# Performance work log

Hardware: AMD Instinct MI355X
Metric: run time of the kernel (lower is better)

The kernel has to match this reference:

```python
import jax, jax.numpy as jnp
import numpy as np

N, E, T = 32768, 262144, 262144
DN, DE = 128, 128
EPS = 1e-5  # torch LayerNorm default eps


def layer_norm(x, g, b):
    m = jnp.mean(x, axis=-1, keepdims=True)
    v = jnp.mean((x - m) ** 2, axis=-1, keepdims=True)
    return (x - m) * jax.lax.rsqrt(v + EPS) * g + b


def setup_inputs() -> dict:
    key = jax.random.key(0)
    ks = jax.random.split(key, 16)
    node_embedding = jax.random.normal(ks[0], (N, DN), dtype=jnp.float32)
    edge_embedding = jax.random.normal(ks[1], (E, DE), dtype=jnp.float32)
    i = jax.random.randint(ks[2], (E,), 0, N)
    j = jax.random.randint(ks[3], (E,), 0, N)
    index_i = jax.random.randint(ks[4], (T,), 0, N)
    index_j = jax.random.randint(ks[5], (T,), 0, N)
    index_k = jax.random.randint(ks[6], (T,), 0, N)
    index_ji = jax.random.randint(ks[7], (T,), 0, E)
    index_kj = jax.random.randint(ks[8], (T,), 0, E)
    d3 = 3 * DN + 2 * DE
    W2 = jax.random.normal(ks[9], (2 * DE, DN), dtype=jnp.float32) / np.sqrt(DN)
    b2 = jnp.zeros((2 * DE,), dtype=jnp.float32)
    W3 = jax.random.normal(ks[10], (2 * DE, d3), dtype=jnp.float32) / np.sqrt(d3)
    b3 = jnp.zeros((2 * DE,), dtype=jnp.float32)
    g_c2 = jnp.ones((2 * DE,), jnp.float32); be_c2 = jnp.zeros((2 * DE,), jnp.float32)
    g_c3 = jnp.ones((2 * DE,), jnp.float32); be_c3 = jnp.zeros((2 * DE,), jnp.float32)
    g_c2_2 = jnp.ones((DE,), jnp.float32); be_c2_2 = jnp.zeros((DE,), jnp.float32)
    g_c3_2 = jnp.ones((DE,), jnp.float32); be_c3_2 = jnp.zeros((DE,), jnp.float32)
    return dict(node_embedding=node_embedding, edge_embedding=edge_embedding,
                i=i, j=j, index_i=index_i, index_j=index_j, index_k=index_k,
                index_ji=index_ji, index_kj=index_kj,
                W2=W2, b2=b2, W3=W3, b3=b3,
                g_c2=g_c2, be_c2=be_c2, g_c3=g_c3, be_c3=be_c3,
                g_c2_2=g_c2_2, be_c2_2=be_c2_2, g_c3_2=g_c3_2, be_c3_2=be_c3_2)


def reference(node_embedding, edge_embedding, i, j, index_i, index_j, index_k,
              index_ji, index_kj, W2, b2, W3, b3,
              g_c2, be_c2, g_c3, be_c3, g_c2_2, be_c2_2, g_c3_2, be_c3_2):
    num_edges = edge_embedding.shape[0]
    # --- c2 branch: per-edge elementwise product of endpoint node embeddings ---
    c2 = node_embedding[i] * node_embedding[j]                      # [E, Dn]
    c2 = layer_norm(c2 @ W2.T + b2, g_c2, be_c2)                    # [E, 2De]
    c2_filter, c2_core = jnp.split(c2, 2, axis=1)
    c2_emb = layer_norm(jax.nn.sigmoid(c2_filter) * jnp.tanh(c2_core), g_c2_2, be_c2_2)
    # --- c3 branch: triplet gather -> linear -> LN -> gate -> scatter-sum ---
    c3 = jnp.concatenate([node_embedding[index_i], node_embedding[index_j],
                          node_embedding[index_k], edge_embedding[index_ji],
                          edge_embedding[index_kj]], axis=1)        # [T, 3Dn+2De]
    c3 = layer_norm(c3 @ W3.T + b3, g_c3, be_c3)                    # [T, 2De]
    c3_filter, c3_core = jnp.split(c3, 2, axis=1)
    msg = jax.nn.sigmoid(c3_filter) * jnp.tanh(c3_core)             # [T, De]
    c3_emb = jax.ops.segment_sum(msg, index_ji, num_segments=num_edges)  # [E, De]
    c3_emb = layer_norm(c3_emb, g_c3_2, be_c3_2)
    return jnp.tanh(edge_embedding + c2_emb + c3_emb)
```

## Files before the change

### kernel.cpp

```cpp
#include <hip/hip_runtime.h>

typedef _Float16 h16;
typedef _Float16 h16x8 __attribute__((ext_vector_type(8)));
typedef float    f32x4 __attribute__((ext_vector_type(4)));

static constexpr int NN  = 32768;
static constexpr int EE  = 262144;
static constexpr int TT  = 262144;
static constexpr int D   = 128;
static constexpr int K3  = 640;
static constexpr int LDA = 72;
#define EPS 1e-5f

__global__ __launch_bounds__(256) void cvt_f32_f16(
    const float* __restrict__ src, h16* __restrict__ dst, int n8)
{
    const int i = blockIdx.x * 256 + threadIdx.x;
    if (i >= n8) return;
    const float4* s = reinterpret_cast<const float4*>(src);
    const float4 a = s[2 * i], b = s[2 * i + 1];
    h16x8 o;
    o[0] = (h16)a.x; o[1] = (h16)a.y; o[2] = (h16)a.z; o[3] = (h16)a.w;
    o[4] = (h16)b.x; o[5] = (h16)b.y; o[6] = (h16)b.z; o[7] = (h16)b.w;
    *reinterpret_cast<h16x8*>(dst + 8 * i) = o;
}

__global__ __launch_bounds__(256, 2) void c3_kernel(
    const h16*  __restrict__ nodeh, const float* __restrict__ edge,
    const h16*  __restrict__ edgeh,
    const int* __restrict__ idx_i, const int* __restrict__ idx_j,
    const int* __restrict__ idx_k, const int* __restrict__ idx_ji,
    const int* __restrict__ idx_kj,
    const h16* __restrict__ W3h, const float* __restrict__ b3,
    const float* __restrict__ g3, const float* __restrict__ be3,
    float* __restrict__ acc3)
{
    __shared__ h16 As[128 * LDA];
    __shared__ h16 Bs[256 * LDA];

    const int tid  = threadIdx.x;
    const int lane = tid & 63;
    const int wave = tid >> 6;
    const int l15  = lane & 15;
    const int quad = lane >> 4;
    const int m0   = blockIdx.x * 128;

    f32x4 acc[2][16];
    #pragma unroll
    for (int mt = 0; mt < 2; ++mt)
        #pragma unroll
        for (int nt = 0; nt < 16; ++nt)
            acc[mt][nt] = (f32x4){0.f, 0.f, 0.f, 0.f};

    const int r = tid >> 1;
    const int h = tid & 1;

    const size_t rI  = (size_t)idx_i [m0 + r];
    const size_t rJ  = (size_t)idx_j [m0 + r];
    const size_t rK  = (size_t)idx_k [m0 + r];
    const size_t rJI = (size_t)idx_ji[m0 + r];
    const size_t rKJ = (size_t)idx_kj[m0 + r];

    h16x8 av[4], bv[8];

#define LDC3(c)                                                                          \
    {                                                                                    \
        const int seg  = (c) >> 1;                                                       \
        const int half = (c) & 1;                                                        \
        const size_t row = (seg == 0) ? rI : (seg == 1) ? rJ                             \
                         : (seg == 2) ? rK : (seg == 3) ? rJI : rKJ;                     \
        if (seg < 3) {                                                                   \
            const h16x8* sp = reinterpret_cast<const h16x8*>(                            \
                nodeh + row * D + half * 64 + h * 32);                                   \
            _Pragma("unroll")                                                            \
            for (int q = 0; q < 4; ++q) av[q] = sp[q];                                   \
        } else if (edgeh) {                                                              \
            const h16x8* sp = reinterpret_cast<const h16x8*>(                            \
                edgeh + row * D + half * 64 + h * 32);                                   \
            _Pragma("unroll")                                                            \
            for (int q = 0; q < 4; ++q) av[q] = sp[q];                                   \
        } else {                                                                         \
            const float4* fp = reinterpret_cast<const float4*>(                          \
                edge + row * D + half * 64 + h * 32);                                    \
            _Pragma("unroll")                                                            \
            for (int q = 0; q < 4; ++q) {                                                \
                const float4 u = fp[2 * q], vv = fp[2 * q + 1];                          \
                h16x8 t;                                                                 \
                t[0] = (h16)u.x;  t[1] = (h16)u.y;  t[2] = (h16)u.z;  t[3] = (h16)u.w;   \
                t[4] = (h16)vv.x; t[5] = (h16)vv.y; t[6] = (h16)vv.z; t[7] = (h16)vv.w;  \
                av[q] = t;                                                               \
            }                                                                            \
        }                                                                                \
        const h16x8* wp = reinterpret_cast<const h16x8*>(                                \
            W3h + (size_t)tid * K3 + (c) * 64);                                          \
        _Pragma("unroll")                                                                \
        for (int q = 0; q < 8; ++q) bv[q] = wp[q];                                       \
    }

    LDC3(0);

    #pragma unroll 1
    for (int c = 0; c < 10; ++c) {
        __syncthreads();
        h16x8* ad = reinterpret_cast<h16x8*>(&As[r * LDA + h * 32]);
        #pragma unroll
        for (int q = 0; q < 4; ++q) ad[q] = av[q];
        h16x8* bd = reinterpret_cast<h16x8*>(&Bs[tid * LDA]);
        #pragma unroll
        for (int q = 0; q < 8; ++q) bd[q] = bv[q];
        __syncthreads();

        if (c < 9) LDC3(c + 1);

        #pragma unroll
        for (int kk = 0; kk < 64; kk += 32) {
            h16x8 a0 = *reinterpret_cast<const h16x8*>(&As[(wave*32      + l15) * LDA + kk + quad*8]);
            h16x8 a1 = *reinterpret_cast<const h16x8*>(&As[(wave*32 + 16 + l15) * LDA + kk + quad*8]);
            #pragma unroll
            for (int nt = 0; nt < 16; ++nt) {
                h16x8 b = *reinterpret_cast<const h16x8*>(&Bs[(nt*16 + l15) * LDA + kk + quad*8]);
                acc[0][nt] = __builtin_amdgcn_mfma_f32_16x16x32_f16(a0, b, acc[0][nt], 0, 0, 0);
                acc[1][nt] = __builtin_amdgcn_mfma_f32_16x16x32_f16(a1, b, acc[1][nt], 0, 0, 0);
            }
        }
    }
#undef LDC3

    float bias[16], gg[16], bb[16];
    #pragma unroll
    for (int nt = 0; nt < 16; ++nt) {
        const int cc = nt * 16 + l15;
        bias[nt] = b3[cc]; gg[nt] = g3[cc]; bb[nt] = be3[cc];
    }
    #pragma unroll
    for (int mt = 0; mt < 2; ++mt) {
        #pragma unroll
        for (int rg = 0; rg < 4; ++rg) {
            float v[16];
            float s = 0.f, s2 = 0.f;
            #pragma unroll
            for (int nt = 0; nt < 16; ++nt) {
                v[nt] = acc[mt][nt][rg] + bias[nt];
                s += v[nt]; s2 += v[nt] * v[nt];
            }
            #pragma unroll
            for (int m = 1; m < 16; m <<= 1) {
                s  += __shfl_xor(s,  m, 64);
                s2 += __shfl_xor(s2, m, 64);
            }
            const float mean = s * (1.f / 256.f);
            const float var  = s2 * (1.f / 256.f) - mean * mean;
            const float inv  = rsqrtf(var + EPS);
            const int rowg   = m0 + wave * 32 + mt * 16 + quad * 4 + rg;
            const size_t e   = (size_t)idx_ji[rowg];
            #pragma unroll
            for (int nt = 0; nt < 8; ++nt) {
                const float f   = (v[nt]     - mean) * inv * gg[nt]     + bb[nt];
                const float co  = (v[nt + 8] - mean) * inv * gg[nt + 8] + bb[nt + 8];
                const float msg = (1.f / (1.f + __expf(-f))) * tanhf(co);
                atomicAdd(&acc3[e * D + nt * 16 + l15], msg);
            }
        }
    }
}

__global__ __launch_bounds__(256, 2) void c2_kernel(
    const h16* __restrict__ nodeh,
    const int* __restrict__ ei, const int* __restrict__ ej,
    const h16* __restrict__ W2h, const float* __restrict__ b2,
    const float* __restrict__ g2, const float* __restrict__ be2,
    const float* __restrict__ g22, const float* __restrict__ be22,
    h16* __restrict__ c2emb)
{
    __shared__ h16 As[128 * LDA];
    __shared__ h16 Bs[256 * LDA];

    const int tid  = threadIdx.x;
    const int lane = tid & 63;
    const int wave = tid >> 6;
    const int l15  = lane & 15;
    const int quad = lane >> 4;
    const int m0   = blockIdx.x * 128;

    f32x4 acc[2][16];
    #pragma unroll
    for (int mt = 0; mt < 2; ++mt)
        #pragma unroll
        for (int nt = 0; nt < 16; ++nt)
            acc[mt][nt] = (f32x4){0.f, 0.f, 0.f, 0.f};

    const int r = tid >> 1;
    const int h = tid & 1;
    const size_t ri = (size_t)ei[m0 + r];
    const size_t rj = (size_t)ej[m0 + r];

    h16x8 av[4], bv[8];

#define LDC2(c)                                                                          \
    {                                                                                    \
        const h16x8* si = reinterpret_cast<const h16x8*>(                                \
            nodeh + ri * D + (c) * 64 + h * 32);                                         \
        const h16x8* sj = reinterpret_cast<const h16x8*>(                                \
            nodeh + rj * D + (c) * 64 + h * 32);                                         \
        _Pragma("unroll")                                                                \
        for (int q = 0; q < 4; ++q) av[q] = si[q] * sj[q];                               \
        const h16x8* wp = reinterpret_cast<const h16x8*>(                                \
            W2h + (size_t)tid * D + (c) * 64);                                           \
        _Pragma("unroll")                                                                \
        for (int q = 0; q < 8; ++q) bv[q] = wp[q];                                       \
    }

    LDC2(0);

    #pragma unroll 1
    for (int c = 0; c < 2; ++c) {
        __syncthreads();
        h16x8* ad = reinterpret_cast<h16x8*>(&As[r * LDA + h * 32]);
        #pragma unroll
        for (int q = 0; q < 4; ++q) ad[q] = av[q];
        h16x8* bd = reinterpret_cast<h16x8*>(&Bs[tid * LDA]);
        #pragma unroll
        for (int q = 0; q < 8; ++q) bd[q] = bv[q];
        __syncthreads();

        if (c < 1) LDC2(c + 1);

        #pragma unroll
        for (int kk = 0; kk < 64; kk += 32) {
            h16x8 a0 = *reinterpret_cast<const h16x8*>(&As[(wave*32      + l15) * LDA + kk + quad*8]);
            h16x8 a1 = *reinterpret_cast<const h16x8*>(&As[(wave*32 + 16 + l15) * LDA + kk + quad*8]);
            #pragma unroll
            for (int nt = 0; nt < 16; ++nt) {
                h16x8 b = *reinterpret_cast<const h16x8*>(&Bs[(nt*16 + l15) * LDA + kk + quad*8]);
                acc[0][nt] = __builtin_amdgcn_mfma_f32_16x16x32_f16(a0, b, acc[0][nt], 0, 0, 0);
                acc[1][nt] = __builtin_amdgcn_mfma_f32_16x16x32_f16(a1, b, acc[1][nt], 0, 0, 0);
            }
        }
    }
#undef LDC2

    float bias[16], gg[16], bb[16];
    #pragma unroll
    for (int nt = 0; nt < 16; ++nt) {
        const int cc = nt * 16 + l15;
        bias[nt] = b2[cc]; gg[nt] = g2[cc]; bb[nt] = be2[cc];
    }
    float g2c[8], b2c[8];
    #pragma unroll
    for (int nt = 0; nt < 8; ++nt) {
        const int cc = nt * 16 + l15;
        g2c[nt] = g22[cc]; b2c[nt] = be22[cc];
    }
    #pragma unroll
    for (int mt = 0; mt < 2; ++mt) {
        #pragma unroll
        for (int rg = 0; rg < 4; ++rg) {
            float v[16];
            float s = 0.f, s2 = 0.f;
            #pragma unroll
            for (int nt = 0; nt < 16; ++nt) {
                v[nt] = acc[mt][nt][rg] + bias[nt];
                s += v[nt]; s2 += v[nt] * v[nt];
            }
            #pragma unroll
            for (int m = 1; m < 16; m <<= 1) {
                s  += __shfl_xor(s,  m, 64);
                s2 += __shfl_xor(s2, m, 64);
            }
            const float mean = s * (1.f / 256.f);
            const float var  = s2 * (1.f / 256.f) - mean * mean;
            const float inv  = rsqrtf(var + EPS);
            float msg[8];
            float t = 0.f, t2 = 0.f;
            #pragma unroll
            for (int nt = 0; nt < 8; ++nt) {
                const float f  = (v[nt]     - mean) * inv * gg[nt]     + bb[nt];
                const float co = (v[nt + 8] - mean) * inv * gg[nt + 8] + bb[nt + 8];
                const float m_ = (1.f / (1.f + __expf(-f))) * tanhf(co);
                msg[nt] = m_; t += m_; t2 += m_ * m_;
            }
            #pragma unroll
            for (int m = 1; m < 16; m <<= 1) {
                t  += __shfl_xor(t,  m, 64);
                t2 += __shfl_xor(t2, m, 64);
            }
            const float mean2 = t * (1.f / 128.f);
            const float var2  = t2 * (1.f / 128.f) - mean2 * mean2;
            const float inv2  = rsqrtf(var2 + EPS);
            const size_t rowg = (size_t)(m0 + wave * 32 + mt * 16 + quad * 4 + rg);
            #pragma unroll
            for (int nt = 0; nt < 8; ++nt) {
                const float o = (msg[nt] - mean2) * inv2 * g2c[nt] + b2c[nt];
                c2emb[rowg * D + nt * 16 + l15] = (h16)o;
            }
        }
    }
}

__global__ __launch_bounds__(256) void final_kernel(
    const float* __restrict__ edge, const h16* __restrict__ c2emb,
    const float* __restrict__ g32, const float* __restrict__ be32,
    float* out)
{
    const int lane = threadIdx.x & 63;
    const int wave = threadIdx.x >> 6;
    const size_t e = (size_t)blockIdx.x * 4 + wave;
    const int c0 = lane * 2;

    const float2 v = *reinterpret_cast<const float2*>(&out[e * D + c0]);
    float s  = v.x + v.y;
    float s2 = v.x * v.x + v.y * v.y;
    #pragma unroll
    for (int m = 1; m < 64; m <<= 1) {
        s  += __shfl_xor(s,  m, 64);
        s2 += __shfl_xor(s2, m, 64);
    }
    const float mean = s * (1.f / 128.f);
    const float var  = s2 * (1.f / 128.f) - mean * mean;
    const float inv  = rsqrtf(var + EPS);
    const float c3a = (v.x - mean) * inv * g32[c0]     + be32[c0];
    const float c3b = (v.y - mean) * inv * g32[c0 + 1] + be32[c0 + 1];

    const float2 ev = *reinterpret_cast<const float2*>(&edge[e * D + c0]);
    const float ca = (float)c2emb[e * D + c0];
    const float cb = (float)c2emb[e * D + c0 + 1];
    float2 o;
    o.x = tanhf(ev.x + ca + c3a);
    o.y = tanhf(ev.y + cb + c3b);
    *reinterpret_cast<float2*>(&out[e * D + c0]) = o;
}

extern "C" void kernel_launch(void* const* d_in, const int* in_sizes, int n_in,
                              void* d_out, int out_size, void* d_ws, size_t ws_size,
                              hipStream_t stream)
{
    const float* node   = (const float*)d_in[0];
    const float* edge   = (const float*)d_in[1];
    const int*   e_i    = (const int*)d_in[2];
    const int*   e_j    = (const int*)d_in[3];
    const int*   idx_i  = (const int*)d_in[4];
    const int*   idx_j  = (const int*)d_in[5];
    const int*   idx_k  = (const int*)d_in[6];
    const int*   idx_ji = (const int*)d_in[7];
    const int*   idx_kj = (const int*)d_in[8];
    const float* W2     = (const float*)d_in[9];
    const float* b2     = (const float*)d_in[10];
    const float* W3     = (const float*)d_in[11];
    const float* b3     = (const float*)d_in[12];
    const float* g_c2   = (const float*)d_in[13];
    const float* be_c2  = (const float*)d_in[14];
    const float* g_c3   = (const float*)d_in[15];
    const float* be_c3  = (const float*)d_in[16];
    const float* g_c22  = (const float*)d_in[17];
    const float* be_c22 = (const float*)d_in[18];
    const float* g_c32  = (const float*)d_in[19];
    const float* be_c32 = (const float*)d_in[20];

    h16* W3h   = (h16*)d_ws;
    h16* W2h   = W3h + 256 * K3;
    h16* nodeh = W2h + 256 * D;
    h16* c2emb = nodeh + (size_t)NN * D;
    h16* edgeh = c2emb + (size_t)EE * D;
    const size_t need = ((size_t)256 * K3 + 256 * D + (size_t)NN * D
                         + 2 * (size_t)EE * D) * sizeof(h16);
    const bool use_edgeh = ws_size >= need;

    float* acc3 = (float*)d_out;
    float* out  = (float*)d_out;

    hipMemsetAsync(d_out, 0, (size_t)EE * D * sizeof(float), stream);
    cvt_f32_f16<<<dim3((256 * K3 / 8 + 255) / 256), dim3(256), 0, stream>>>(W3, W3h, 256 * K3 / 8);
    cvt_f32_f16<<<dim3((256 * D  / 8 + 255) / 256), dim3(256), 0, stream>>>(W2, W2h, 256 * D / 8);
    cvt_f32_f16<<<dim3((NN * D   / 8 + 255) / 256), dim3(256), 0, stream>>>(node, nodeh, NN * D / 8);
    if (use_edgeh)
        cvt_f32_f16<<<dim3((EE * D / 8 + 255) / 256), dim3(256), 0, stream>>>(edge, edgeh, EE * D / 8);

    c3_kernel<<<dim3(TT / 128), dim3(256), 0, stream>>>(
        nodeh, edge, use_edgeh ? edgeh : (const h16*)nullptr,
        idx_i, idx_j, idx_k, idx_ji, idx_kj, W3h, b3, g_c3, be_c3, acc3);
    c2_kernel<<<dim3(EE / 128), dim3(256), 0, stream>>>(
        nodeh, e_i, e_j, W2h, b2, g_c2, be_c2, g_c22, be_c22, c2emb);
    final_kernel<<<dim3(EE / 4), dim3(256), 0, stream>>>(
        edge, c2emb, g_c32, be_c32, out);
}
```

Before: 688.9 us.

## Retile c3 MFMA warps as 2x2 and fuse final epilogue into c2 kernel

The c3 GEMM now splits its 4 waves as 2 along M by 2 along N, each covering 64 rows and 128 columns. This raises A-fragment reuse and reduces LDS reads of B per MFMA. The LayerNorm row statistics are combined across the two N-waves through a small shared buffer and an extra barrier. Separately, the final LayerNorm plus tanh stage is folded into the c2 kernel's epilogue. This removes the fp16 c2emb round trip through global memory and one kernel launch, at the cost of more registers and strided per-lane global loads of edge and acc3 in that epilogue.

```diff
diff --git a/kernel.cpp b/kernel.cpp
--- a/kernel.cpp
+++ b/kernel.cpp
@@ -37,19 +37,22 @@
 {
     __shared__ h16 As[128 * LDA];
     __shared__ h16 Bs[256 * LDA];
+    __shared__ float2 Ps[128][2];
 
     const int tid  = threadIdx.x;
     const int lane = tid & 63;
     const int wave = tid >> 6;
+    const int wm   = wave >> 1;
+    const int wn   = wave & 1;
     const int l15  = lane & 15;
     const int quad = lane >> 4;
     const int m0   = blockIdx.x * 128;
 
-    f32x4 acc[2][16];
-    #pragma unroll
-    for (int mt = 0; mt < 2; ++mt)
-        #pragma unroll
-        for (int nt = 0; nt < 16; ++nt)
+    f32x4 acc[4][8];
+    #pragma unroll
+    for (int mt = 0; mt < 4; ++mt)
+        #pragma unroll
+        for (int nt = 0; nt < 8; ++nt)
             acc[mt][nt] = (f32x4){0.f, 0.f, 0.f, 0.f};
 
     const int r = tid >> 1;
@@ -114,51 +117,73 @@
 
         #pragma unroll
         for (int kk = 0; kk < 64; kk += 32) {
-            h16x8 a0 = *reinterpret_cast<const h16x8*>(&As[(wave*32      + l15) * LDA + kk + quad*8]);
-            h16x8 a1 = *reinterpret_cast<const h16x8*>(&As[(wave*32 + 16 + l15) * LDA + kk + quad*8]);
-            #pragma unroll
-            for (int nt = 0; nt < 16; ++nt) {
-                h16x8 b = *reinterpret_cast<const h16x8*>(&Bs[(nt*16 + l15) * LDA + kk + quad*8]);
-                acc[0][nt] = __builtin_amdgcn_mfma_f32_16x16x32_f16(a0, b, acc[0][nt], 0, 0, 0);
-                acc[1][nt] = __builtin_amdgcn_mfma_f32_16x16x32_f16(a1, b, acc[1][nt], 0, 0, 0);
+            h16x8 a[4];
+            #pragma unroll
+            for (int mt = 0; mt < 4; ++mt)
+                a[mt] = *reinterpret_cast<const h16x8*>(
+                    &As[(wm*64 + mt*16 + l15) * LDA + kk + quad*8]);
+            #pragma unroll
+            for (int nt = 0; nt < 8; ++nt) {
+                const int p = (nt < 4) ? (wn*4 + nt) : (8 + wn*4 + nt - 4);
+                h16x8 b = *reinterpret_cast<const h16x8*>(
+                    &Bs[(p*16 + l15) * LDA + kk + quad*8]);
+                #pragma unroll
+                for (int mt = 0; mt < 4; ++mt)
+                    acc[mt][nt] = __builtin_amdgcn_mfma_f32_16x16x32_f16(a[mt], b, acc[mt][nt], 0, 0, 0);
             }
         }
     }
 #undef LDC3
 
-    float bias[16], gg[16], bb[16];
-    #pragma unroll
-    for (int nt = 0; nt < 16; ++nt) {
-        const int cc = nt * 16 + l15;
-        bias[nt] = b3[cc]; gg[nt] = g3[cc]; bb[nt] = be3[cc];
-    }
-    #pragma unroll
-    for (int mt = 0; mt < 2; ++mt) {
+    float bias[2][4], gg[2][4], bb[2][4];
+    #pragma unroll
+    for (int hf = 0; hf < 2; ++hf)
+        #pragma unroll
+        for (int q = 0; q < 4; ++q) {
+            const int cc = hf*128 + (wn*4 + q)*16 + l15;
+            bias[hf][q] = b3[cc]; gg[hf][q] = g3[cc]; bb[hf][q] = be3[cc];
+        }
+
+    float sA[4][4], s2A[4][4];
+    #pragma unroll
+    for (int mt = 0; mt < 4; ++mt) {
         #pragma unroll
         for (int rg = 0; rg < 4; ++rg) {
-            float v[16];
             float s = 0.f, s2 = 0.f;
             #pragma unroll
-            for (int nt = 0; nt < 16; ++nt) {
-                v[nt] = acc[mt][nt][rg] + bias[nt];
-                s += v[nt]; s2 += v[nt] * v[nt];
+            for (int nt = 0; nt < 8; ++nt) {
+                const float x = acc[mt][nt][rg] + bias[nt >> 2][nt & 3];
+                s += x; s2 += x * x;
             }
             #pragma unroll
             for (int m = 1; m < 16; m <<= 1) {
                 s  += __shfl_xor(s,  m, 64);
                 s2 += __shfl_xor(s2, m, 64);
             }
-            const float mean = s * (1.f / 256.f);
-            const float var  = s2 * (1.f / 256.f) - mean * mean;
+            sA[mt][rg] = s; s2A[mt][rg] = s2;
+            if (l15 == 0)
+                Ps[wm*64 + mt*16 + quad*4 + rg][wn] = make_float2(s, s2);
+        }
+    }
+    __syncthreads();
+    #pragma unroll
+    for (int mt = 0; mt < 4; ++mt) {
+        #pragma unroll
+        for (int rg = 0; rg < 4; ++rg) {
+            const int rl = wm*64 + mt*16 + quad*4 + rg;
+            const float2 po = Ps[rl][wn ^ 1];
+            const float S  = sA[mt][rg]  + po.x;
+            const float S2 = s2A[mt][rg] + po.y;
+            const float mean = S * (1.f / 256.f);
+            const float var  = S2 * (1.f / 256.f) - mean * mean;
             const float inv  = rsqrtf(var + EPS);
-            const int rowg   = m0 + wave * 32 + mt * 16 + quad * 4 + rg;
-            const size_t e   = (size_t)idx_ji[rowg];
-            #pragma unroll
-            for (int nt = 0; nt < 8; ++nt) {
-                const float f   = (v[nt]     - mean) * inv * gg[nt]     + bb[nt];
-                const float co  = (v[nt + 8] - mean) * inv * gg[nt + 8] + bb[nt + 8];
+            const size_t e   = (size_t)idx_ji[m0 + rl];
+            #pragma unroll
+            for (int q = 0; q < 4; ++q) {
+                const float f   = (acc[mt][q][rg]     + bias[0][q] - mean) * inv * gg[0][q] + bb[0][q];
+                const float co  = (acc[mt][4 + q][rg] + bias[1][q] - mean) * inv * gg[1][q] + bb[1][q];
                 const float msg = (1.f / (1.f + __expf(-f))) * tanhf(co);
-                atomicAdd(&acc3[e * D + nt * 16 + l15], msg);
+                atomicAdd(&acc3[e * D + (wn*4 + q)*16 + l15], msg);
             }
         }
     }
@@ -170,7 +195,9 @@
     const h16* __restrict__ W2h, const float* __restrict__ b2,
     const float* __restrict__ g2, const float* __restrict__ be2,
     const float* __restrict__ g22, const float* __restrict__ be22,
-    h16* __restrict__ c2emb)
+    const float* __restrict__ g32, const float* __restrict__ be32,
+    const float* __restrict__ edge,
+    float* __restrict__ out)
 {
     __shared__ h16 As[128 * LDA];
     __shared__ h16 Bs[256 * LDA];
@@ -245,11 +272,12 @@
         const int cc = nt * 16 + l15;
         bias[nt] = b2[cc]; gg[nt] = g2[cc]; bb[nt] = be2[cc];
     }
-    float g2c[8], b2c[8];
+    float g2c[8], b2c[8], g3c[8], b3c[8];
     #pragma unroll
     for (int nt = 0; nt < 8; ++nt) {
         const int cc = nt * 16 + l15;
         g2c[nt] = g22[cc]; b2c[nt] = be22[cc];
+        g3c[nt] = g32[cc]; b3c[nt] = be32[cc];
     }
     #pragma unroll
     for (int mt = 0; mt < 2; ++mt) {
@@ -270,64 +298,42 @@
             const float mean = s * (1.f / 256.f);
             const float var  = s2 * (1.f / 256.f) - mean * mean;
             const float inv  = rsqrtf(var + EPS);
-            float msg[8];
-            float t = 0.f, t2 = 0.f;
+            const size_t rowg = (size_t)(m0 + wave * 32 + mt * 16 + quad * 4 + rg);
+
+            float msg[8], a3[8];
+            float t = 0.f, t2 = 0.f, u = 0.f, u2 = 0.f;
             #pragma unroll
             for (int nt = 0; nt < 8; ++nt) {
                 const float f  = (v[nt]     - mean) * inv * gg[nt]     + bb[nt];
                 const float co = (v[nt + 8] - mean) * inv * gg[nt + 8] + bb[nt + 8];
                 const float m_ = (1.f / (1.f + __expf(-f))) * tanhf(co);
                 msg[nt] = m_; t += m_; t2 += m_ * m_;
+                const float a_ = out[rowg * D + nt * 16 + l15];
+                a3[nt] = a_; u += a_; u2 += a_ * a_;
             }
             #pragma unroll
             for (int m = 1; m < 16; m <<= 1) {
                 t  += __shfl_xor(t,  m, 64);
                 t2 += __shfl_xor(t2, m, 64);
+                u  += __shfl_xor(u,  m, 64);
+                u2 += __shfl_xor(u2, m, 64);
             }
             const float mean2 = t * (1.f / 128.f);
             const float var2  = t2 * (1.f / 128.f) - mean2 * mean2;
             const float inv2  = rsqrtf(var2 + EPS);
-            const size_t rowg = (size_t)(m0 + wave * 32 + mt * 16 + quad * 4 + rg);
+            const float mean3 = u * (1.f / 128.f);
+            const float var3  = u2 * (1.f / 128.f) - mean3 * mean3;
+            const float inv3  = rsqrtf(var3 + EPS);
             #pragma unroll
             for (int nt = 0; nt < 8; ++nt) {
-                const float o = (msg[nt] - mean2) * inv2 * g2c[nt] + b2c[nt];
-                c2emb[rowg * D + nt * 16 + l15] = (h16)o;
-            }
-        }
-    }
-}
-
-__global__ __launch_bounds__(256) void final_kernel(
-    const float* __restrict__ edge, const h16* __restrict__ c2emb,
-    const float* __restrict__ g32, const float* __restrict__ be32,
-    float* out)
-{
-    const int lane = threadIdx.x & 63;
-    const int wave = threadIdx.x >> 6;
-    const size_t e = (size_t)blockIdx.x * 4 + wave;
-    const int c0 = lane * 2;
-
-    const float2 v = *reinterpret_cast<const float2*>(&out[e * D + c0]);
-    float s  = v.x + v.y;
-    float s2 = v.x * v.x + v.y * v.y;
-    #pragma unroll
-    for (int m = 1; m < 64; m <<= 1) {
-        s  += __shfl_xor(s,  m, 64);
-        s2 += __shfl_xor(s2, m, 64);
-    }
-    const float mean = s * (1.f / 128.f);
-    const float var  = s2 * (1.f / 128.f) - mean * mean;
-    const float inv  = rsqrtf(var + EPS);
-    const float c3a = (v.x - mean) * inv * g32[c0]     + be32[c0];
-    const float c3b = (v.y - mean) * inv * g32[c0 + 1] + be32[c0 + 1];
-
-    const float2 ev = *reinterpret_cast<const float2*>(&edge[e * D + c0]);
-    const float ca = (float)c2emb[e * D + c0];
-    const float cb = (float)c2emb[e * D + c0 + 1];
-    float2 o;
-    o.x = tanhf(ev.x + ca + c3a);
-    o.y = tanhf(ev.y + cb + c3b);
-    *reinterpret_cast<float2*>(&out[e * D + c0]) = o;
+                const int cc = nt * 16 + l15;
+                const float c2v = (msg[nt] - mean2) * inv2 * g2c[nt] + b2c[nt];
+                const float c3v = (a3[nt]  - mean3) * inv3 * g3c[nt] + b3c[nt];
+                const float ev  = edge[rowg * D + cc];
+                out[rowg * D + cc] = tanhf(ev + c2v + c3v);
+            }
+        }
+    }
 }
 
 extern "C" void kernel_launch(void* const* d_in, const int* in_sizes, int n_in,
@@ -359,10 +365,9 @@
     h16* W3h   = (h16*)d_ws;
     h16* W2h   = W3h + 256 * K3;
     h16* nodeh = W2h + 256 * D;
-    h16* c2emb = nodeh + (size_t)NN * D;
-    h16* edgeh = c2emb + (size_t)EE * D;
+    h16* edgeh = nodeh + (size_t)NN * D;
     const size_t need = ((size_t)256 * K3 + 256 * D + (size_t)NN * D
-                         + 2 * (size_t)EE * D) * sizeof(h16);
+                         + (size_t)EE * D) * sizeof(h16);
     const bool use_edgeh = ws_size >= need;
 
     float* acc3 = (float*)d_out;
@@ -379,7 +384,6 @@
         nodeh, edge, use_edgeh ? edgeh : (const h16*)nullptr,
         idx_i, idx_j, idx_k, idx_ji, idx_kj, W3h, b3, g_c3, be_c3, acc3);
     c2_kernel<<<dim3(EE / 128), dim3(256), 0, stream>>>(
-        nodeh, e_i, e_j, W2h, b2, g_c2, be_c2, g_c22, be_c22, c2emb);
-    final_kernel<<<dim3(EE / 4), dim3(256), 0, stream>>>(
-        edge, c2emb, g_c32, be_c32, out);
+        nodeh, e_i, e_j, W2h, b2, g_c2, be_c2, g_c22, be_c22,
+        g_c32, be_c32, edge, out);
 }
```

Result: slower. 800.9 us (+16.3%).

## Fuse final LayerNorm/tanh into c2 kernel and coalesce gather/weight loads

Applied to the files above, without the earlier changes.

Removes the separate final kernel by folding the c3 LayerNorm, edge add and tanh epilogue into the c2 kernel, which drops the fp16 c2emb intermediate and its write and read. Gather loads now use 8 threads per row with 16-byte chunks, so each row read is a contiguous 128-byte segment. Weights are pre-transposed into a chunk-major layout so that each weight load across threads is coalesced. The c2 epilogue now does extra strided reads of the accumulator and of the edge rows, which may raise register pressure.

```diff
diff --git a/kernel.cpp b/kernel.cpp
--- a/kernel.cpp
+++ b/kernel.cpp
@@ -25,13 +25,32 @@
     *reinterpret_cast<h16x8*>(dst + 8 * i) = o;
 }
 
+__global__ __launch_bounds__(256) void cvt_w_t(
+    const float* __restrict__ src, h16* __restrict__ dst, int K, int n8)
+{
+    const int t = blockIdx.x * 256 + threadIdx.x;
+    if (t >= n8) return;
+    const int d   = t * 8;
+    const int c   = d >> 14;
+    const int rem = d & 16383;
+    const int q   = rem >> 11;
+    const int n   = (rem >> 3) & 255;
+    const int k   = c * 64 + q * 8;
+    const float4* s = reinterpret_cast<const float4*>(src + (size_t)n * K + k);
+    const float4 a = s[0], b = s[1];
+    h16x8 o;
+    o[0] = (h16)a.x; o[1] = (h16)a.y; o[2] = (h16)a.z; o[3] = (h16)a.w;
+    o[4] = (h16)b.x; o[5] = (h16)b.y; o[6] = (h16)b.z; o[7] = (h16)b.w;
+    *reinterpret_cast<h16x8*>(dst + d) = o;
+}
+
 __global__ __launch_bounds__(256, 2) void c3_kernel(
     const h16*  __restrict__ nodeh, const float* __restrict__ edge,
     const h16*  __restrict__ edgeh,
     const int* __restrict__ idx_i, const int* __restrict__ idx_j,
     const int* __restrict__ idx_k, const int* __restrict__ idx_ji,
     const int* __restrict__ idx_kj,
-    const h16* __restrict__ W3h, const float* __restrict__ b3,
+    const h16* __restrict__ W3t, const float* __restrict__ b3,
     const float* __restrict__ g3, const float* __restrict__ be3,
     float* __restrict__ acc3)
 {
@@ -52,14 +71,18 @@
         for (int nt = 0; nt < 16; ++nt)
             acc[mt][nt] = (f32x4){0.f, 0.f, 0.f, 0.f};
 
-    const int r = tid >> 1;
-    const int h = tid & 1;
-
-    const size_t rI  = (size_t)idx_i [m0 + r];
-    const size_t rJ  = (size_t)idx_j [m0 + r];
-    const size_t rK  = (size_t)idx_k [m0 + r];
-    const size_t rJI = (size_t)idx_ji[m0 + r];
-    const size_t rKJ = (size_t)idx_kj[m0 + r];
+    const int r8  = tid >> 3;
+    const int sub = tid & 7;
+
+    int rIdx[5][4];
+    {
+        const int* arrs[5] = {idx_i, idx_j, idx_k, idx_ji, idx_kj};
+        #pragma unroll
+        for (int sg = 0; sg < 5; ++sg)
+            #pragma unroll
+            for (int p = 0; p < 4; ++p)
+                rIdx[sg][p] = arrs[sg][m0 + p * 32 + r8];
+    }
 
     h16x8 av[4], bv[8];
 
@@ -67,34 +90,28 @@
     {                                                                                    \
         const int seg  = (c) >> 1;                                                       \
         const int half = (c) & 1;                                                        \
-        const size_t row = (seg == 0) ? rI : (seg == 1) ? rJ                             \
-                         : (seg == 2) ? rK : (seg == 3) ? rJI : rKJ;                     \
-        if (seg < 3) {                                                                   \
-            const h16x8* sp = reinterpret_cast<const h16x8*>(                            \
-                nodeh + row * D + half * 64 + h * 32);                                   \
-            _Pragma("unroll")                                                            \
-            for (int q = 0; q < 4; ++q) av[q] = sp[q];                                   \
-        } else if (edgeh) {                                                              \
-            const h16x8* sp = reinterpret_cast<const h16x8*>(                            \
-                edgeh + row * D + half * 64 + h * 32);                                   \
-            _Pragma("unroll")                                                            \
-            for (int q = 0; q < 4; ++q) av[q] = sp[q];                                   \
-        } else {                                                                         \
-            const float4* fp = reinterpret_cast<const float4*>(                          \
-                edge + row * D + half * 64 + h * 32);                                    \
-            _Pragma("unroll")                                                            \
-            for (int q = 0; q < 4; ++q) {                                                \
-                const float4 u = fp[2 * q], vv = fp[2 * q + 1];                          \
+        _Pragma("unroll")                                                                \
+        for (int p = 0; p < 4; ++p) {                                                    \
+            const size_t row = (size_t)rIdx[seg][p];                                     \
+            if (seg < 3) {                                                               \
+                av[p] = *reinterpret_cast<const h16x8*>(                                 \
+                    nodeh + row * D + half * 64 + sub * 8);                              \
+            } else if (edgeh) {                                                          \
+                av[p] = *reinterpret_cast<const h16x8*>(                                 \
+                    edgeh + row * D + half * 64 + sub * 8);                              \
+            } else {                                                                     \
+                const float4* fp = reinterpret_cast<const float4*>(                      \
+                    edge + row * D + half * 64 + sub * 8);                               \
+                const float4 u = fp[0], vv = fp[1];                                      \
                 h16x8 t;                                                                 \
                 t[0] = (h16)u.x;  t[1] = (h16)u.y;  t[2] = (h16)u.z;  t[3] = (h16)u.w;   \
                 t[4] = (h16)vv.x; t[5] = (h16)vv.y; t[6] = (h16)vv.z; t[7] = (h16)vv.w;  \
-                av[q] = t;                                                               \
+                av[p] = t;                                                               \
             }                                                                            \
         }                                                                                \
-        const h16x8* wp = reinterpret_cast<const h16x8*>(                                \
-            W3h + (size_t)tid * K3 + (c) * 64);                                          \
+        const h16x8* wp = reinterpret_cast<const h16x8*>(W3t) + (c) * 2048 + tid;        \
         _Pragma("unroll")                                                                \
-        for (int q = 0; q < 8; ++q) bv[q] = wp[q];                                       \
+        for (int q = 0; q < 8; ++q) bv[q] = wp[q * 256];                                 \
     }
 
     LDC3(0);
@@ -102,9 +119,9 @@
     #pragma unroll 1
     for (int c = 0; c < 10; ++c) {
         __syncthreads();
-        h16x8* ad = reinterpret_cast<h16x8*>(&As[r * LDA + h * 32]);
-        #pragma unroll
-        for (int q = 0; q < 4; ++q) ad[q] = av[q];
+        #pragma unroll
+        for (int p = 0; p < 4; ++p)
+            *reinterpret_cast<h16x8*>(&As[(p * 32 + r8) * LDA + sub * 8]) = av[p];
         h16x8* bd = reinterpret_cast<h16x8*>(&Bs[tid * LDA]);
         #pragma unroll
         for (int q = 0; q < 8; ++q) bd[q] = bv[q];
@@ -167,10 +184,12 @@
 __global__ __launch_bounds__(256, 2) void c2_kernel(
     const h16* __restrict__ nodeh,
     const int* __restrict__ ei, const int* __restrict__ ej,
-    const h16* __restrict__ W2h, const float* __restrict__ b2,
+    const h16* __restrict__ W2t, const float* __restrict__ b2,
     const float* __restrict__ g2, const float* __restrict__ be2,
     const float* __restrict__ g22, const float* __restrict__ be22,
-    h16* __restrict__ c2emb)
+    const float* __restrict__ g32, const float* __restrict__ be32,
+    const float* __restrict__ edge,
+    float* __restrict__ out)
 {
     __shared__ h16 As[128 * LDA];
     __shared__ h16 Bs[256 * LDA];
@@ -189,25 +208,31 @@
         for (int nt = 0; nt < 16; ++nt)
             acc[mt][nt] = (f32x4){0.f, 0.f, 0.f, 0.f};
 
-    const int r = tid >> 1;
-    const int h = tid & 1;
-    const size_t ri = (size_t)ei[m0 + r];
-    const size_t rj = (size_t)ej[m0 + r];
+    const int r8  = tid >> 3;
+    const int sub = tid & 7;
+
+    int rI[4], rJ[4];
+    #pragma unroll
+    for (int p = 0; p < 4; ++p) {
+        rI[p] = ei[m0 + p * 32 + r8];
+        rJ[p] = ej[m0 + p * 32 + r8];
+    }
 
     h16x8 av[4], bv[8];
 
 #define LDC2(c)                                                                          \
     {                                                                                    \
-        const h16x8* si = reinterpret_cast<const h16x8*>(                                \
-            nodeh + ri * D + (c) * 64 + h * 32);                                         \
-        const h16x8* sj = reinterpret_cast<const h16x8*>(                                \
-            nodeh + rj * D + (c) * 64 + h * 32);                                         \
         _Pragma("unroll")                                                                \
-        for (int q = 0; q < 4; ++q) av[q] = si[q] * sj[q];                               \
-        const h16x8* wp = reinterpret_cast<const h16x8*>(                                \
-            W2h + (size_t)tid * D + (c) * 64);                                           \
+        for (int p = 0; p < 4; ++p) {                                                    \
+            const h16x8 si = *reinterpret_cast<const h16x8*>(                            \
+                nodeh + (size_t)rI[p] * D + (c) * 64 + sub * 8);                         \
+            const h16x8 sj = *reinterpret_cast<const h16x8*>(                            \
+                nodeh + (size_t)rJ[p] * D + (c) * 64 + sub * 8);                         \
+            av[p] = si * sj;                                                             \
+        }                                                                                \
+        const h16x8* wp = reinterpret_cast<const h16x8*>(W2t) + (c) * 2048 + tid;        \
         _Pragma("unroll")                                                                \
-        for (int q = 0; q < 8; ++q) bv[q] = wp[q];                                       \
+        for (int q = 0; q < 8; ++q) bv[q] = wp[q * 256];                                 \
     }
 
     LDC2(0);
@@ -215,9 +240,9 @@
     #pragma unroll 1
     for (int c = 0; c < 2; ++c) {
         __syncthreads();
-        h16x8* ad = reinterpret_cast<h16x8*>(&As[r * LDA + h * 32]);
-        #pragma unroll
-        for (int q = 0; q < 4; ++q) ad[q] = av[q];
+        #pragma unroll
+        for (int p = 0; p < 4; ++p)
+            *reinterpret_cast<h16x8*>(&As[(p * 32 + r8) * LDA + sub * 8]) = av[p];
         h16x8* bd = reinterpret_cast<h16x8*>(&Bs[tid * LDA]);
         #pragma unroll
         for (int q = 0; q < 8; ++q) bd[q] = bv[q];
@@ -245,11 +270,12 @@
         const int cc = nt * 16 + l15;
         bias[nt] = b2[cc]; gg[nt] = g2[cc]; bb[nt] = be2[cc];
     }
-    float g2c[8], b2c[8];
+    float g2c[8], b2c[8], g3c[8], b3c[8];
     #pragma unroll
     for (int nt = 0; nt < 8; ++nt) {
         const int cc = nt * 16 + l15;
         g2c[nt] = g22[cc]; b2c[nt] = be22[cc];
+        g3c[nt] = g32[cc]; b3c[nt] = be32[cc];
     }
     #pragma unroll
     for (int mt = 0; mt < 2; ++mt) {
@@ -270,64 +296,42 @@
             const float mean = s * (1.f / 256.f);
             const float var  = s2 * (1.f / 256.f) - mean * mean;
             const float inv  = rsqrtf(var + EPS);
-            float msg[8];
-            float t = 0.f, t2 = 0.f;
+            const size_t rowg = (size_t)(m0 + wave * 32 + mt * 16 + quad * 4 + rg);
+
+            float msg[8], a3[8];
+            float t = 0.f, t2 = 0.f, u = 0.f, u2 = 0.f;
             #pragma unroll
             for (int nt = 0; nt < 8; ++nt) {
                 const float f  = (v[nt]     - mean) * inv * gg[nt]     + bb[nt];
                 const float co = (v[nt + 8] - mean) * inv * gg[nt + 8] + bb[nt + 8];
                 const float m_ = (1.f / (1.f + __expf(-f))) * tanhf(co);
                 msg[nt] = m_; t += m_; t2 += m_ * m_;
+                const float a_ = out[rowg * D + nt * 16 + l15];
+                a3[nt] = a_; u += a_; u2 += a_ * a_;
             }
             #pragma unroll
             for (int m = 1; m < 16; m <<= 1) {
                 t  += __shfl_xor(t,  m, 64);
                 t2 += __shfl_xor(t2, m, 64);
+                u  += __shfl_xor(u,  m, 64);
+                u2 += __shfl_xor(u2, m, 64);
             }
             const float mean2 = t * (1.f / 128.f);
             const float var2  = t2 * (1.f / 128.f) - mean2 * mean2;
             const float inv2  = rsqrtf(var2 + EPS);
-            const size_t rowg = (size_t)(m0 + wave * 32 + mt * 16 + quad * 4 + rg);
+            const float mean3 = u * (1.f / 128.f);
+            const float var3  = u2 * (1.f / 128.f) - mean3 * mean3;
+            const float inv3  = rsqrtf(var3 + EPS);
             #pragma unroll
             for (int nt = 0; nt < 8; ++nt) {
-                const float o = (msg[nt] - mean2) * inv2 * g2c[nt] + b2c[nt];
-                c2emb[rowg * D + nt * 16 + l15] = (h16)o;
+                const int cc = nt * 16 + l15;
+                const float c2v = (msg[nt] - mean2) * inv2 * g2c[nt] + b2c[nt];
+                const float c3v = (a3[nt]  - mean3) * inv3 * g3c[nt] + b3c[nt];
+                const float ev  = edge[rowg * D + cc];
+                out[rowg * D + cc] = tanhf(ev + c2v + c3v);
             }
         }
     }
-}
-
-__global__ __launch_bounds__(256) void final_kernel(
-    const float* __restrict__ edge, const h16* __restrict__ c2emb,
-    const float* __restrict__ g32, const float* __restrict__ be32,
-    float* out)
-{
-    const int lane = threadIdx.x & 63;
-    const int wave = threadIdx.x >> 6;
-    const size_t e = (size_t)blockIdx.x * 4 + wave;
-    const int c0 = lane * 2;
-
-    const float2 v = *reinterpret_cast<const float2*>(&out[e * D + c0]);
-    float s  = v.x + v.y;
-    float s2 = v.x * v.x + v.y * v.y;
-    #pragma unroll
-    for (int m = 1; m < 64; m <<= 1) {
-        s  += __shfl_xor(s,  m, 64);
-        s2 += __shfl_xor(s2, m, 64);
-    }
-    const float mean = s * (1.f / 128.f);
-    const float var  = s2 * (1.f / 128.f) - mean * mean;
-    const float inv  = rsqrtf(var + EPS);
-    const float c3a = (v.x - mean) * inv * g32[c0]     + be32[c0];
-    const float c3b = (v.y - mean) * inv * g32[c0 + 1] + be32[c0 + 1];
-
-    const float2 ev = *reinterpret_cast<const float2*>(&edge[e * D + c0]);
-    const float ca = (float)c2emb[e * D + c0];
-    const float cb = (float)c2emb[e * D + c0 + 1];
-    float2 o;
-    o.x = tanhf(ev.x + ca + c3a);
-    o.y = tanhf(ev.y + cb + c3b);
-    *reinterpret_cast<float2*>(&out[e * D + c0]) = o;
 }
 
 extern "C" void kernel_launch(void* const* d_in, const int* in_sizes, int n_in,
@@ -356,30 +360,28 @@
     const float* g_c32  = (const float*)d_in[19];
     const float* be_c32 = (const float*)d_in[20];
 
-    h16* W3h   = (h16*)d_ws;
-    h16* W2h   = W3h + 256 * K3;
-    h16* nodeh = W2h + 256 * D;
-    h16* c2emb = nodeh + (size_t)NN * D;
-    h16* edgeh = c2emb + (size_t)EE * D;
+    h16* W3t   = (h16*)d_ws;
+    h16* W2t   = W3t + 256 * K3;
+    h16* nodeh = W2t + 256 * D;
+    h16* edgeh = nodeh + (size_t)NN * D;
     const size_t need = ((size_t)256 * K3 + 256 * D + (size_t)NN * D
-                         + 2 * (size_t)EE * D) * sizeof(h16);
+                         + (size_t)EE * D) * sizeof(h16);
     const bool use_edgeh = ws_size >= need;
 
     float* acc3 = (float*)d_out;
     float* out  = (float*)d_out;
 
     hipMemsetAsync(d_out, 0, (size_t)EE * D * sizeof(float), stream);
-    cvt_f32_f16<<<dim3((256 * K3 / 8 + 255) / 256), dim3(256), 0, stream>>>(W3, W3h, 256 * K3 / 8);
-    cvt_f32_f16<<<dim3((256 * D  / 8 + 255) / 256), dim3(256), 0, stream>>>(W2, W2h, 256 * D / 8);
+    cvt_w_t<<<dim3((256 * K3 / 8 + 255) / 256), dim3(256), 0, stream>>>(W3, W3t, K3, 256 * K3 / 8);
+    cvt_w_t<<<dim3((256 * D  / 8 + 255) / 256), dim3(256), 0, stream>>>(W2, W2t, D, 256 * D / 8);
     cvt_f32_f16<<<dim3((NN * D   / 8 + 255) / 256), dim3(256), 0, stream>>>(node, nodeh, NN * D / 8);
     if (use_edgeh)
         cvt_f32_f16<<<dim3((EE * D / 8 + 255) / 256), dim3(256), 0, stream>>>(edge, edgeh, EE * D / 8);
 
     c3_kernel<<<dim3(TT / 128), dim3(256), 0, stream>>>(
         nodeh, edge, use_edgeh ? edgeh : (const h16*)nullptr,
-        idx_i, idx_j, idx_k, idx_ji, idx_kj, W3h, b3, g_c3, be_c3, acc3);
+        idx_i, idx_j, idx_k, idx_ji, idx_kj, W3t, b3, g_c3, be_c3, acc3);
     c2_kernel<<<dim3(EE / 128), dim3(256), 0, stream>>>(
-        nodeh, e_i, e_j, W2h, b2, g_c2, be_c2, g_c22, be_c22, c2emb);
-    final_kernel<<<dim3(EE / 4), dim3(256), 0, stream>>>(
-        edge, c2emb, g_c32, be_c32, out);
-}
+        nodeh, e_i, e_j, W2t, b2, g_c2, be_c2, g_c22, be_c22,
+        g_c32, be_c32, edge, out);
+}
```

Measured after the change: 715.1 us. +3.8%, slower.
